# Kernel optimization log

Measured on AMD Instinct MI355X. Metric: run time of the kernel, lower is better.

Reference implementation:

```python
import jax, jax.numpy as jnp
import numpy as np

N, B, D, Q = 32, 36, 2048, 1024  # batch, objects, v_dim, q_dim


def setup_inputs() -> dict:
    key = jax.random.key(0)
    ks = jax.random.split(key, 6)
    sc = 0.02  # small init so ReLU chains stay well-scaled
    return {
        "v": jax.random.normal(ks[0], (N, B, D), jnp.float32),
        "q": jax.random.normal(ks[1], (N, Q), jnp.float32),
        "W1": jax.random.normal(ks[2], (D, D), jnp.float32) * sc,
        "b1": jnp.zeros((D,), jnp.float32),
        "W2": jax.random.normal(ks[3], (D, D), jnp.float32) * sc,
        "b2": jnp.zeros((D,), jnp.float32),
        "W3": jax.random.normal(ks[4], (Q, D), jnp.float32) * sc,
        "b3": jnp.zeros((D,), jnp.float32),
    }


def reference(v, q, W1, b1, W2, b2, W3, b3):
    # FCNet = ReLU(Linear(.)) with weight-norm folded, dropout=0 (eval).
    # Original calls linear3 twice (linear4 unused bug), so q_emb == q_emb2.
    qe = jax.nn.relu(q @ W3 + b3)  # (N, D)
    # pairs[n,i,j] = v[n,i]*qe[n] + v[n,j]*qe[n]  -> (N, B, B, D)
    pairs = (v[:, :, None, :] + v[:, None, :, :]) * qe[:, None, None, :]
    h = jax.nn.relu(jnp.einsum('nijd,de->nije', pairs, W1) + b1)  # linear1
    x = jnp.sum(h, axis=2)  # sum over j relations -> (N, B, D)
    return jax.nn.relu(x @ W2 + b2)  # linear2
```

## Files before the change

kernel.cpp:

```cpp
#include <hip/hip_runtime.h>
#include <stdint.h>

#define N_BATCH 32
#define B_OBJ   36
#define D_DIM   2048
#define Q_DIM   1024

typedef __bf16 bf16x8 __attribute__((ext_vector_type(8)));
typedef float  f32x4  __attribute__((ext_vector_type(4)));

__device__ __forceinline__ uint16_t f2bf(float f) {
    uint32_t u = __builtin_bit_cast(uint32_t, f);
    uint32_t r = (u + 0x7FFFu + ((u >> 16) & 1u)) >> 16;
    return (uint16_t)r;
}

__device__ __forceinline__ void gld_lds16(const void* g, void* l) {
    __builtin_amdgcn_global_load_lds(
        (const __attribute__((address_space(1))) uint32_t*)g,
        (__attribute__((address_space(3))) uint32_t*)l, 16, 0, 0);
}

__global__ __launch_bounds__(256) void transpose_all(
    const float* __restrict__ W1, const float* __restrict__ W2,
    const float* __restrict__ W3,
    uint16_t* __restrict__ W1t, uint16_t* __restrict__ W2t,
    uint16_t* __restrict__ W3t) {
    __shared__ float tile[64][65];
    int gy = blockIdx.y;
    const float* W; uint16_t* Wt; int K, k0;
    if (gy < 32)      { W = W1; Wt = W1t; K = 2048; k0 = gy * 64; }
    else if (gy < 64) { W = W2; Wt = W2t; K = 2048; k0 = (gy - 32) * 64; }
    else              { W = W3; Wt = W3t; K = 1024; k0 = (gy - 64) * 64; }
    int n0 = blockIdx.x * 64;
    int t = threadIdx.x;
    {
        int r = t >> 4, c = (t & 15) * 4;
#pragma unroll
        for (int p = 0; p < 4; ++p)
            *(float4*)&tile[r + p * 16][c] =
                *(const float4*)&W[(size_t)(k0 + r + p * 16) * 2048 + n0 + c];
    }
    __syncthreads();
    {
        int n = t >> 2, kb = (t & 3) * 16;
#pragma unroll
        for (int g4 = 0; g4 < 4; ++g4) {
            int k = kb + g4 * 4;
            ushort4 o;
            o.x = f2bf(tile[k][n]);     o.y = f2bf(tile[k + 1][n]);
            o.z = f2bf(tile[k + 2][n]); o.w = f2bf(tile[k + 3][n]);
            *(ushort4*)&Wt[(size_t)(n0 + n) * K + k0 + k] = o;
        }
    }
}

__global__ __launch_bounds__(256) void qk_gemm(
    const float* __restrict__ q,
    const uint16_t* __restrict__ W3t,
    float* __restrict__ qpart) {
    __shared__ __align__(16) uint16_t As[32][32];
    __shared__ __align__(16) uint16_t Bs[128][32];
    int t = threadIdx.x, lane = t & 63, wave = t >> 6;
    int l15 = lane & 15, quad = lane >> 4;
    int n0 = blockIdx.x * 128;
    int kbase = blockIdx.y * 256;
    f32x4 acc[2][2] = {};
    int ar = t >> 3, ac = (t & 7) * 4;
    int br = t >> 2, bk = (t & 3) * 8;

    for (int k0 = 0; k0 < 256; k0 += 32) {
        __syncthreads();
        float4 av = *(const float4*)&q[(size_t)ar * Q_DIM + kbase + k0 + ac];
        ushort4 a4;
        a4.x = f2bf(av.x); a4.y = f2bf(av.y); a4.z = f2bf(av.z); a4.w = f2bf(av.w);
        *(ushort4*)&As[ar][ac] = a4;
        *(uint4*)&Bs[br][bk]      = *(const uint4*)&W3t[(size_t)(n0 + br) * Q_DIM + kbase + k0 + bk];
        *(uint4*)&Bs[br + 64][bk] = *(const uint4*)&W3t[(size_t)(n0 + br + 64) * Q_DIM + kbase + k0 + bk];
        __syncthreads();
        bf16x8 af[2], bfr[2];
        af[0]  = *(const bf16x8*)&As[l15][quad * 8];
        af[1]  = *(const bf16x8*)&As[16 + l15][quad * 8];
        bfr[0] = *(const bf16x8*)&Bs[wave * 32 + l15][quad * 8];
        bfr[1] = *(const bf16x8*)&Bs[wave * 32 + 16 + l15][quad * 8];
#pragma unroll
        for (int i = 0; i < 2; ++i)
#pragma unroll
            for (int j = 0; j < 2; ++j)
                acc[i][j] = __builtin_amdgcn_mfma_f32_16x16x32_bf16(af[i], bfr[j], acc[i][j], 0, 0, 0);
    }
    float* dst = qpart + (size_t)blockIdx.y * 32 * D_DIM;
#pragma unroll
    for (int i = 0; i < 2; ++i)
#pragma unroll
        for (int j = 0; j < 2; ++j) {
            int n = n0 + wave * 32 + j * 16 + l15;
#pragma unroll
            for (int r = 0; r < 4; ++r)
                dst[(size_t)(i * 16 + quad * 4 + r) * D_DIM + n] = acc[i][j][r];
        }
}

__global__ void qe_reduce(const float* __restrict__ qpart,
                          const float* __restrict__ b3,
                          float* __restrict__ qe) {
    int i = blockIdx.x * 256 + threadIdx.x;
    const float4* p = (const float4*)qpart;
    float4 s = p[i];
    float4 s1 = p[16384 + i], s2 = p[32768 + i], s3 = p[49152 + i];
    float4 b = ((const float4*)b3)[i & 511];
    float4 o;
    o.x = fmaxf(s.x + s1.x + s2.x + s3.x + b.x, 0.f);
    o.y = fmaxf(s.y + s1.y + s2.y + s3.y + b.y, 0.f);
    o.z = fmaxf(s.z + s1.z + s2.z + s3.z + b.z, 0.f);
    o.w = fmaxf(s.w + s1.w + s2.w + s3.w + b.w, 0.f);
    ((float4*)qe)[i] = o;
}

__global__ void make_u(const float* __restrict__ v,
                       const float* __restrict__ qe,
                       uint16_t* __restrict__ u) {
    int idx = blockIdx.x * 256 + threadIdx.x;
    const int total = (N_BATCH * B_OBJ * D_DIM) / 4;
    if (idx >= total) return;
    int d4 = idx % (D_DIM / 4);
    int nb = idx / ((B_OBJ * D_DIM) / 4);
    float4 vv = ((const float4*)v)[idx];
    float4 qq = ((const float4*)qe)[(size_t)nb * (D_DIM / 4) + d4];
    ushort4 o;
    o.x = f2bf(vv.x * qq.x);
    o.y = f2bf(vv.y * qq.y);
    o.z = f2bf(vv.z * qq.z);
    o.w = f2bf(vv.w * qq.w);
    ((ushort4*)u)[idx] = o;
}

__global__ __launch_bounds__(256) void gemm_batch(
    const uint16_t* __restrict__ A,
    const uint16_t* __restrict__ Bt,
    const float* __restrict__ bias,
    void* __restrict__ Cv,
    int mode) {
    __shared__ __align__(16) float smemf[6336];
    uint16_t* As = (uint16_t*)smemf;
    uint16_t* Bs = As + 3072;
    float* yt = smemf;

    int t = threadIdx.x, lane = t & 63, wave = t >> 6;
    int l15 = lane & 15, quad = lane >> 4;
    int nb = blockIdx.y;
    int n0 = blockIdx.x * 128;
    const uint16_t* Ab = A + (size_t)nb * B_OBJ * D_DIM;

    const uint16_t* gp[6]; uint16_t* lp[6];
#pragma unroll
    for (int c = 0; c < 6; ++c) {
        int r = wave + 4 * c;
        int rr = (r < 22) ? r : 0;
        if (rr < 6) {
            int h = rr / 3, g = rr % 3;
            int row = g * 16 + (lane >> 2), kk = h * 32 + (lane & 3) * 8;
            gp[c] = Ab + (size_t)row * D_DIM + kk;
            lp[c] = As + h * 1536 + g * 512;
        } else {
            int rb = rr - 6, h = rb >> 3, g = rb & 7;
            int row = g * 16 + (lane >> 2), kk = h * 32 + (lane & 3) * 8;
            gp[c] = Bt + (size_t)(n0 + row) * D_DIM + kk;
            lp[c] = Bs + h * 4096 + g * 512;
        }
    }

    f32x4 acc[3][2] = {};

    for (int k0 = 0; k0 < D_DIM; k0 += 64) {
        __syncthreads();
#pragma unroll
        for (int c = 0; c < 6; ++c)
            if (wave + 4 * c < 22) gld_lds16(gp[c] + k0, lp[c]);
        __syncthreads();
#pragma unroll
        for (int s = 0; s < 2; ++s) {
            bf16x8 af[3], bfr[2];
#pragma unroll
            for (int i = 0; i < 3; ++i)
                af[i] = *(const bf16x8*)(As + s * 1536 + (i * 16 + l15) * 32 + quad * 8);
#pragma unroll
            for (int j = 0; j < 2; ++j)
                bfr[j] = *(const bf16x8*)(Bs + s * 4096 + (wave * 32 + j * 16 + l15) * 32 + quad * 8);
#pragma unroll
            for (int i = 0; i < 3; ++i)
#pragma unroll
                for (int j = 0; j < 2; ++j)
                    acc[i][j] = __builtin_amdgcn_mfma_f32_16x16x32_bf16(af[i], bfr[j], acc[i][j], 0, 0, 0);
        }
    }

    if (mode == 0) {
        uint16_t* X = (uint16_t*)Cv;
        __syncthreads();
#pragma unroll
        for (int i = 0; i < 3; ++i)
#pragma unroll
            for (int j = 0; j < 2; ++j)
#pragma unroll
                for (int r = 0; r < 4; ++r)
                    yt[(i * 16 + quad * 4 + r) * 132 + wave * 32 + j * 16 + l15] = acc[i][j][r];
        __syncthreads();
        int col = t & 127, half = t >> 7;
        float b = bias[n0 + col];
        float z[36];
#pragma unroll
        for (int j = 0; j < 36; ++j) z[j] = yt[j * 132 + col];
#pragma unroll
        for (int ii = 0; ii < 18; ++ii) {
            int i = half * 18 + ii;
            float zi = z[i] + b;
            float s = 0.f;
#pragma unroll
            for (int j = 0; j < 36; ++j) s += fmaxf(zi + z[j], 0.f);
            X[(size_t)(nb * B_OBJ + i) * D_DIM + n0 + col] = f2bf(s);
        }
    } else {
        float* O = (float*)Cv;
#pragma unroll
        for (int i = 0; i < 3; ++i)
#pragma unroll
            for (int r = 0; r < 4; ++r) {
                int row = i * 16 + quad * 4 + r;
                if (row < B_OBJ) {
#pragma unroll
                    for (int j = 0; j < 2; ++j) {
                        int cc = n0 + wave * 32 + j * 16 + l15;
                        O[(size_t)(nb * B_OBJ + row) * D_DIM + cc] =
                            fmaxf(acc[i][j][r] + bias[cc], 0.f);
                    }
                }
            }
    }
}

extern "C" void kernel_launch(void* const* d_in, const int* in_sizes, int n_in,
                              void* d_out, int out_size, void* d_ws, size_t ws_size,
                              hipStream_t stream) {
    const float* v  = (const float*)d_in[0];
    const float* q  = (const float*)d_in[1];
    const float* W1 = (const float*)d_in[2];
    const float* b1 = (const float*)d_in[3];
    const float* W2 = (const float*)d_in[4];
    const float* b2 = (const float*)d_in[5];
    const float* W3 = (const float*)d_in[6];
    const float* b3 = (const float*)d_in[7];
    float* out = (float*)d_out;

    char* ws = (char*)d_ws;
    uint16_t* W1t   = (uint16_t*)(ws + 0);
    uint16_t* W2t   = (uint16_t*)(ws + 8388608);
    uint16_t* W3t   = (uint16_t*)(ws + 16777216);
    uint16_t* u     = (uint16_t*)(ws + 16777216);
    float*    qpart = (float*)   (ws + 21495808);
    float*    qe    = (float*)   (ws + 22544384);
    uint16_t* x     = (uint16_t*)(ws + 22806528);

    transpose_all<<<dim3(32, 80), 256, 0, stream>>>(W1, W2, W3, W1t, W2t, W3t);

    qk_gemm<<<dim3(16, 4), 256, 0, stream>>>(q, W3t, qpart);
    qe_reduce<<<64, 256, 0, stream>>>(qpart, b3, qe);

    make_u<<<(N_BATCH * B_OBJ * D_DIM / 4 + 255) / 256, 256, 0, stream>>>(v, qe, u);

    gemm_batch<<<dim3(16, N_BATCH), 256, 0, stream>>>(u, W1t, b1, x, 0);

    gemm_batch<<<dim3(16, N_BATCH), 256, 0, stream>>>(x, W2t, b2, out, 1);
}
```

Baseline: 179.0 us.

## Fuse qe reduction into u construction and tile two batches per GEMM block

Merges the qe bias/ReLU reduction with the v*qe bf16 conversion into one kernel, so qe is no longer written to and reread from memory and one launch disappears. Each block of the batched GEMM now covers two batches (72 rows padded to 80 instead of 36 padded to 48) and takes a K step of 128. This cuts the MFMA work wasted on padding and doubles reuse of each loaded W tile. In exchange the GEMM grid halves to 256 blocks, LDS use rises to about 53KB, and the fused elementwise kernel runs on only 64 blocks, which may limit its memory bandwidth.

```diff
diff --git a/kernel.cpp b/kernel.cpp
--- a/kernel.cpp
+++ b/kernel.cpp
@@ -101,38 +101,30 @@
         }
 }
 
-__global__ void qe_reduce(const float* __restrict__ qpart,
-                          const float* __restrict__ b3,
-                          float* __restrict__ qe) {
-    int i = blockIdx.x * 256 + threadIdx.x;
+__global__ __launch_bounds__(256) void qe_makeu(
+    const float* __restrict__ qpart, const float* __restrict__ b3,
+    const float* __restrict__ v, uint16_t* __restrict__ u) {
+    int n = blockIdx.y;
+    int c4 = blockIdx.x * 256 + threadIdx.x;
     const float4* p = (const float4*)qpart;
-    float4 s = p[i];
-    float4 s1 = p[16384 + i], s2 = p[32768 + i], s3 = p[49152 + i];
-    float4 b = ((const float4*)b3)[i & 511];
-    float4 o;
-    o.x = fmaxf(s.x + s1.x + s2.x + s3.x + b.x, 0.f);
-    o.y = fmaxf(s.y + s1.y + s2.y + s3.y + b.y, 0.f);
-    o.z = fmaxf(s.z + s1.z + s2.z + s3.z + b.z, 0.f);
-    o.w = fmaxf(s.w + s1.w + s2.w + s3.w + b.w, 0.f);
-    ((float4*)qe)[i] = o;
-}
-
-__global__ void make_u(const float* __restrict__ v,
-                       const float* __restrict__ qe,
-                       uint16_t* __restrict__ u) {
-    int idx = blockIdx.x * 256 + threadIdx.x;
-    const int total = (N_BATCH * B_OBJ * D_DIM) / 4;
-    if (idx >= total) return;
-    int d4 = idx % (D_DIM / 4);
-    int nb = idx / ((B_OBJ * D_DIM) / 4);
-    float4 vv = ((const float4*)v)[idx];
-    float4 qq = ((const float4*)qe)[(size_t)nb * (D_DIM / 4) + d4];
-    ushort4 o;
-    o.x = f2bf(vv.x * qq.x);
-    o.y = f2bf(vv.y * qq.y);
-    o.z = f2bf(vv.z * qq.z);
-    o.w = f2bf(vv.w * qq.w);
-    ((ushort4*)u)[idx] = o;
+    size_t base = (size_t)n * 512 + c4;
+    float4 s0 = p[base], s1 = p[16384 + base], s2 = p[32768 + base], s3 = p[49152 + base];
+    float4 b = ((const float4*)b3)[c4];
+    float4 qe;
+    qe.x = fmaxf(s0.x + s1.x + s2.x + s3.x + b.x, 0.f);
+    qe.y = fmaxf(s0.y + s1.y + s2.y + s3.y + b.y, 0.f);
+    qe.z = fmaxf(s0.z + s1.z + s2.z + s3.z + b.z, 0.f);
+    qe.w = fmaxf(s0.w + s1.w + s2.w + s3.w + b.w, 0.f);
+    const float4* v4 = (const float4*)v + (size_t)n * B_OBJ * 512 + c4;
+    ushort4* u4 = (ushort4*)u + (size_t)n * B_OBJ * 512 + c4;
+#pragma unroll 4
+    for (int i = 0; i < B_OBJ; ++i) {
+        float4 vv = v4[(size_t)i * 512];
+        ushort4 o;
+        o.x = f2bf(vv.x * qe.x); o.y = f2bf(vv.y * qe.y);
+        o.z = f2bf(vv.z * qe.z); o.w = f2bf(vv.w * qe.w);
+        u4[(size_t)i * 512] = o;
+    }
 }
 
 __global__ __launch_bounds__(256) void gemm_batch(
@@ -141,54 +133,51 @@
     const float* __restrict__ bias,
     void* __restrict__ Cv,
     int mode) {
-    __shared__ __align__(16) float smemf[6336];
+    __shared__ __align__(16) float smemf[13312];
     uint16_t* As = (uint16_t*)smemf;
-    uint16_t* Bs = As + 3072;
+    uint16_t* Bs = As + 10240;
     float* yt = smemf;
 
     int t = threadIdx.x, lane = t & 63, wave = t >> 6;
     int l15 = lane & 15, quad = lane >> 4;
-    int nb = blockIdx.y;
+    int bg = blockIdx.y;
     int n0 = blockIdx.x * 128;
-    const uint16_t* Ab = A + (size_t)nb * B_OBJ * D_DIM;
-
-    const uint16_t* gp[6]; uint16_t* lp[6];
-#pragma unroll
-    for (int c = 0; c < 6; ++c) {
-        int r = wave + 4 * c;
-        int rr = (r < 22) ? r : 0;
-        if (rr < 6) {
-            int h = rr / 3, g = rr % 3;
-            int row = g * 16 + (lane >> 2), kk = h * 32 + (lane & 3) * 8;
-            gp[c] = Ab + (size_t)row * D_DIM + kk;
-            lp[c] = As + h * 1536 + g * 512;
+    const uint16_t* Ab = A + (size_t)bg * 72 * D_DIM;
+
+    const uint16_t* gp[13]; uint16_t* lp[13];
+#pragma unroll
+    for (int c = 0; c < 13; ++c) {
+        int r = wave * 13 + c;
+        int row16 = lane >> 2, kin = (lane & 3) * 8;
+        if (r < 20) {
+            int h = r / 5, g = r % 5;
+            gp[c] = Ab + (size_t)(g * 16 + row16) * D_DIM + h * 32 + kin;
+            lp[c] = As + h * 2560 + g * 512;
         } else {
-            int rb = rr - 6, h = rb >> 3, g = rb & 7;
-            int row = g * 16 + (lane >> 2), kk = h * 32 + (lane & 3) * 8;
-            gp[c] = Bt + (size_t)(n0 + row) * D_DIM + kk;
+            int rb = r - 20, h = rb >> 3, g = rb & 7;
+            gp[c] = Bt + (size_t)(n0 + g * 16 + row16) * D_DIM + h * 32 + kin;
             lp[c] = Bs + h * 4096 + g * 512;
         }
     }
 
-    f32x4 acc[3][2] = {};
-
-    for (int k0 = 0; k0 < D_DIM; k0 += 64) {
-        __syncthreads();
-#pragma unroll
-        for (int c = 0; c < 6; ++c)
-            if (wave + 4 * c < 22) gld_lds16(gp[c] + k0, lp[c]);
-        __syncthreads();
-#pragma unroll
-        for (int s = 0; s < 2; ++s) {
-            bf16x8 af[3], bfr[2];
-#pragma unroll
-            for (int i = 0; i < 3; ++i)
-                af[i] = *(const bf16x8*)(As + s * 1536 + (i * 16 + l15) * 32 + quad * 8);
+    f32x4 acc[5][2] = {};
+
+    for (int k0 = 0; k0 < D_DIM; k0 += 128) {
+        __syncthreads();
+#pragma unroll
+        for (int c = 0; c < 13; ++c) gld_lds16(gp[c] + k0, lp[c]);
+        __syncthreads();
+#pragma unroll
+        for (int s = 0; s < 4; ++s) {
+            bf16x8 af[5], bfr[2];
+#pragma unroll
+            for (int i = 0; i < 5; ++i)
+                af[i] = *(const bf16x8*)(As + s * 2560 + (i * 16 + l15) * 32 + quad * 8);
 #pragma unroll
             for (int j = 0; j < 2; ++j)
                 bfr[j] = *(const bf16x8*)(Bs + s * 4096 + (wave * 32 + j * 16 + l15) * 32 + quad * 8);
 #pragma unroll
-            for (int i = 0; i < 3; ++i)
+            for (int i = 0; i < 5; ++i)
 #pragma unroll
                 for (int j = 0; j < 2; ++j)
                     acc[i][j] = __builtin_amdgcn_mfma_f32_16x16x32_bf16(af[i], bfr[j], acc[i][j], 0, 0, 0);
@@ -199,42 +188,44 @@
         uint16_t* X = (uint16_t*)Cv;
         __syncthreads();
 #pragma unroll
-        for (int i = 0; i < 3; ++i)
-#pragma unroll
-            for (int j = 0; j < 2; ++j)
-#pragma unroll
-                for (int r = 0; r < 4; ++r)
-                    yt[(i * 16 + quad * 4 + r) * 132 + wave * 32 + j * 16 + l15] = acc[i][j][r];
+        for (int i = 0; i < 5; ++i)
+#pragma unroll
+            for (int r = 0; r < 4; ++r) {
+                int row = i * 16 + quad * 4 + r;
+                if (row < 72)
+#pragma unroll
+                    for (int j = 0; j < 2; ++j)
+                        yt[row * 132 + wave * 32 + j * 16 + l15] = acc[i][j][r];
+            }
         __syncthreads();
         int col = t & 127, half = t >> 7;
         float b = bias[n0 + col];
         float z[36];
 #pragma unroll
-        for (int j = 0; j < 36; ++j) z[j] = yt[j * 132 + col];
-#pragma unroll
-        for (int ii = 0; ii < 18; ++ii) {
-            int i = half * 18 + ii;
-            float zi = z[i] + b;
+        for (int j2 = 0; j2 < 36; ++j2) z[j2] = yt[(half * 36 + j2) * 132 + col];
+        int batch = bg * 2 + half;
+#pragma unroll
+        for (int i2 = 0; i2 < 36; ++i2) {
+            float zi = z[i2] + b;
             float s = 0.f;
 #pragma unroll
-            for (int j = 0; j < 36; ++j) s += fmaxf(zi + z[j], 0.f);
-            X[(size_t)(nb * B_OBJ + i) * D_DIM + n0 + col] = f2bf(s);
+            for (int j2 = 0; j2 < 36; ++j2) s += fmaxf(zi + z[j2], 0.f);
+            X[(size_t)(batch * 36 + i2) * D_DIM + n0 + col] = f2bf(s);
         }
     } else {
         float* O = (float*)Cv;
 #pragma unroll
-        for (int i = 0; i < 3; ++i)
+        for (int i = 0; i < 5; ++i)
 #pragma unroll
             for (int r = 0; r < 4; ++r) {
                 int row = i * 16 + quad * 4 + r;
-                if (row < B_OBJ) {
+                if (row < 72)
 #pragma unroll
                     for (int j = 0; j < 2; ++j) {
                         int cc = n0 + wave * 32 + j * 16 + l15;
-                        O[(size_t)(nb * B_OBJ + row) * D_DIM + cc] =
+                        O[(size_t)(bg * 72 + row) * D_DIM + cc] =
                             fmaxf(acc[i][j][r] + bias[cc], 0.f);
                     }
-                }
             }
     }
 }
@@ -258,17 +249,15 @@
     uint16_t* W3t   = (uint16_t*)(ws + 16777216);
     uint16_t* u     = (uint16_t*)(ws + 16777216);
     float*    qpart = (float*)   (ws + 21495808);
-    float*    qe    = (float*)   (ws + 22544384);
     uint16_t* x     = (uint16_t*)(ws + 22806528);
 
     transpose_all<<<dim3(32, 80), 256, 0, stream>>>(W1, W2, W3, W1t, W2t, W3t);
 
     qk_gemm<<<dim3(16, 4), 256, 0, stream>>>(q, W3t, qpart);
-    qe_reduce<<<64, 256, 0, stream>>>(qpart, b3, qe);
-
-    make_u<<<(N_BATCH * B_OBJ * D_DIM / 4 + 255) / 256, 256, 0, stream>>>(v, qe, u);
-
-    gemm_batch<<<dim3(16, N_BATCH), 256, 0, stream>>>(u, W1t, b1, x, 0);
-
-    gemm_batch<<<dim3(16, N_BATCH), 256, 0, stream>>>(x, W2t, b2, out, 1);
-}
+
+    qe_makeu<<<dim3(2, N_BATCH), 256, 0, stream>>>(qpart, b3, v, u);
+
+    gemm_batch<<<dim3(16, 16), 256, 0, stream>>>(u, W1t, b1, x, 0);
+
+    gemm_batch<<<dim3(16, 16), 256, 0, stream>>>(x, W2t, b2, out, 1);
+}
```

After: 187.9 us. +5.0%, slower.
